# Performance work log

Hardware: AMD Instinct MI355X
Metric: run time of the kernel (lower is better)

The kernel has to match this reference:

```python
import jax, jax.numpy as jnp
import numpy as np

H = 16  # heads
D = 1024  # hidden
HD = D // H
FF = 4096
EPS = 1e-12


def _linear_params(key, d_in, d_out):
    k1, k2 = jax.random.split(key)
    bound = 1.0 / np.sqrt(d_in)
    W = jax.random.uniform(k1, (d_in, d_out), minval=-bound, maxval=bound, dtype=jnp.float32)
    b = jax.random.uniform(k2, (d_out,), minval=-bound, maxval=bound, dtype=jnp.float32)
    return W, b


def setup_inputs() -> dict:
    key = jax.random.key(0)
    ks = jax.random.split(key, 8)
    x = jax.random.normal(ks[0], (4, 2048, D), dtype=jnp.float32)
    mask = jnp.ones((4, 1, 1, 2048), dtype=jnp.int32)
    Wq, bq = _linear_params(ks[1], D, D)
    Wk, bk = _linear_params(ks[2], D, D)
    Wv, bv = _linear_params(ks[3], D, D)
    Wo, bo = _linear_params(ks[4], D, D)
    W1, b1 = _linear_params(ks[5], D, FF)
    W2, b2 = _linear_params(ks[6], FF, D)
    g1 = jnp.ones((D,), jnp.float32); be1 = jnp.zeros((D,), jnp.float32)
    g2 = jnp.ones((D,), jnp.float32); be2 = jnp.zeros((D,), jnp.float32)
    return {"x": x, "mask": mask,
            "Wq": Wq, "bq": bq, "Wk": Wk, "bk": bk, "Wv": Wv, "bv": bv,
            "Wo": Wo, "bo": bo, "W1": W1, "b1": b1, "W2": W2, "b2": b2,
            "g1": g1, "be1": be1, "g2": g2, "be2": be2}


def _layernorm(x, g, b):
    mu = jnp.mean(x, axis=-1, keepdims=True)
    var = jnp.mean(jnp.square(x - mu), axis=-1, keepdims=True)
    return (x - mu) / jnp.sqrt(var + EPS) * g + b


def reference(x, mask, Wq, bq, Wk, bk, Wv, bv, Wo, bo, W1, b1, W2, b2, g1, be1, g2, be2):
    B, L, _ = x.shape
    h = _layernorm(x, g1, be1)
    # [B, H, L, HD]
    q = (h @ Wq + bq).reshape(B, L, H, HD).transpose(0, 2, 1, 3)
    k = (h @ Wk + bk).reshape(B, L, H, HD).transpose(0, 2, 1, 3)
    v = (h @ Wv + bv).reshape(B, L, H, HD).transpose(0, 2, 1, 3)
    scores = jnp.einsum('bhqd,bhkd->bhqk', q, k) / np.sqrt(HD).astype(np.float32)
    scores = jnp.where(mask == 0, jnp.float32(-1e9), scores)
    attn = jax.nn.softmax(scores, axis=-1)  # dropout = identity (eval mode)
    out = jnp.einsum('bhqk,bhkd->bhqd', attn, v)
    out = out.transpose(0, 2, 1, 3).reshape(B, L, D)
    x = x + (out @ Wo + bo)
    h = _layernorm(x, g2, be2)
    ff = jax.nn.gelu(h @ W1 + b1, approximate=False) @ W2 + b2
    return x + ff
```

## Files before the change

### kernel.cpp

```cpp
#include <hip/hip_runtime.h>
#include <stdint.h>

#define D_MODEL 1024
#define NHEAD   16
#define HDIM    64
#define FFDIM   4096
#define BATCH   4
#define SEQ     2048
#define ROWS    (BATCH*SEQ)

typedef unsigned short u16;
typedef __bf16 bf16_t;
typedef bf16_t bf16x8 __attribute__((ext_vector_type(8)));
typedef float  f32x4  __attribute__((ext_vector_type(4)));
typedef float  f32x16 __attribute__((ext_vector_type(16)));

#define SCQ 0.18033688011112042f

__device__ __forceinline__ u16 f2bf(float f) {
  union { float f; unsigned u; } v; v.f = f;
  unsigned r = v.u + 0x7fffu + ((v.u >> 16) & 1u);
  return (u16)(r >> 16);
}

__device__ __forceinline__ void gl2lds16(const void* g, void* l) {
  __builtin_amdgcn_global_load_lds((const __attribute__((address_space(1))) void*)g,
                                   (__attribute__((address_space(3))) void*)l, 16, 0, 0);
}

#define MFMA_BF16(a, b, c) __builtin_amdgcn_mfma_f32_16x16x32_bf16((a), (b), (c), 0, 0, 0)
#define MFMA32(a, b, c)    __builtin_amdgcn_mfma_f32_32x32x16_bf16((a), (b), (c), 0, 0, 0)
#define EXP2(x) __builtin_amdgcn_exp2f(x)

__device__ __forceinline__ bf16x8 mk8(unsigned a, unsigned b, unsigned c, unsigned d) {
  union { unsigned u[4]; bf16x8 v; } t;
  t.u[0] = a; t.u[1] = b; t.u[2] = c; t.u[3] = d;
  return t.v;
}

__global__ __launch_bounds__(256) void ln_kernel(const float* __restrict__ x,
                                                 const float* __restrict__ g,
                                                 const float* __restrict__ be,
                                                 u16* __restrict__ out) {
  __shared__ float red[10];
  int row = blockIdx.x;
  int t = threadIdx.x;
  const float* xr = x + (size_t)row * D_MODEL;
  float4 xv = ((const float4*)xr)[t];
  float s  = xv.x + xv.y + xv.z + xv.w;
  float s2 = xv.x*xv.x + xv.y*xv.y + xv.z*xv.z + xv.w*xv.w;
  for (int d = 32; d > 0; d >>= 1) { s += __shfl_down(s, d); s2 += __shfl_down(s2, d); }
  int wid = t >> 6;
  if ((t & 63) == 0) { red[wid*2] = s; red[wid*2+1] = s2; }
  __syncthreads();
  if (t == 0) {
    float a = 0.f, b2 = 0.f;
    for (int i = 0; i < 4; ++i) { a += red[i*2]; b2 += red[i*2+1]; }
    red[8] = a; red[9] = b2;
  }
  __syncthreads();
  float mu  = red[8] * (1.0f / D_MODEL);
  float var = red[9] * (1.0f / D_MODEL) - mu*mu;
  float rstd = rsqrtf(var + 1e-12f);
  float4 gv = ((const float4*)g)[t];
  float4 bv = ((const float4*)be)[t];
  unsigned long long o =
      (unsigned long long)f2bf((xv.x - mu) * rstd * gv.x + bv.x)
    | ((unsigned long long)f2bf((xv.y - mu) * rstd * gv.y + bv.y) << 16)
    | ((unsigned long long)f2bf((xv.z - mu) * rstd * gv.z + bv.z) << 32)
    | ((unsigned long long)f2bf((xv.w - mu) * rstd * gv.w + bv.w) << 48);
  ((unsigned long long*)out)[(size_t)row * (D_MODEL/4) + t] = o;
}

__global__ __launch_bounds__(256) void wt_kernel(const float* __restrict__ W,
                                                 u16* __restrict__ Wt, int K, int N) {
  __shared__ float tile[32][33];
  int n0 = blockIdx.x * 32, k0 = blockIdx.y * 32;
  int tx = threadIdx.x & 31, ty = threadIdx.x >> 5;
  #pragma unroll
  for (int i = 0; i < 4; ++i) {
    int k = ty + i*8;
    tile[k][tx] = W[(size_t)(k0 + k) * N + n0 + tx];
  }
  __syncthreads();
  #pragma unroll
  for (int i = 0; i < 4; ++i) {
    int n = ty + i*8;
    Wt[(size_t)(n0 + n) * K + k0 + tx] = f2bf(tile[tx][n]);
  }
}

__global__ __launch_bounds__(256) void vtrans_kernel(const u16* __restrict__ vb,
                                                     u16* __restrict__ vt) {
  __shared__ __align__(16) u16 tile[64][80];
  int kb = blockIdx.x * 64;
  int bh = blockIdx.y;
  int b = bh >> 4, h = bh & 15;
  int t = threadIdx.x;
  int key = t >> 2, dq = (t & 3) * 16;
  const u16* src = vb + (size_t)b*SEQ*D_MODEL + (size_t)(kb+key)*D_MODEL + h*HDIM + dq;
  *(bf16x8*)&tile[key][dq]     = *(const bf16x8*)(src);
  *(bf16x8*)&tile[key][dq + 8] = *(const bf16x8*)(src + 8);
  __syncthreads();
  int w = t >> 6, lane = t & 63;
  int kq = w * 16;
  u16 vals[16];
  #pragma unroll
  for (int e = 0; e < 16; ++e) vals[e] = tile[kq + e][lane];
  u16* dst = vt + (size_t)bh * HDIM * SEQ + (size_t)lane * SEQ + kb + kq;
  *(bf16x8*)dst       = *(const bf16x8*)&vals[0];
  *(bf16x8*)(dst + 8) = *(const bf16x8*)&vals[8];
}

__device__ __forceinline__ float gelu_f(float v) {
  return 0.5f * v * (1.0f + erff(v * 0.70710678118654752f));
}

template<int EPI>
__global__ __launch_bounds__(512, 2) void gemm256(const u16* __restrict__ A,
                                                  const u16* __restrict__ Bt,
                                                  const float* __restrict__ bias,
                                                  const float* __restrict__ resid,
                                                  void* __restrict__ outp,
                                                  int M, int N, int K,
                                                  const float* __restrict__ bias2,
                                                  const float* __restrict__ bias3,
                                                  void* __restrict__ out2,
                                                  void* __restrict__ out3) {
  __shared__ __align__(16) u16 sA[3][128*64];
  __shared__ __align__(16) u16 sB[3][256*64];
  const int tid = threadIdx.x;
  const int lane = tid & 63, w = tid >> 6;
  const int r = lane & 15, kg = lane >> 4, r7 = r & 7;
  const int wr = w >> 2, wc = w & 3;

  const int gx = gridDim.x;
  const int nwg = gx * gridDim.y;
  const int orig = blockIdx.y * gx + blockIdx.x;
  const int lid = (orig & 7) * (nwg >> 3) + (orig >> 3);
  const int bm = lid / gx, bn = lid % gx;

  const int NT = K >> 6;

  size_t offA[2], offB[4];
  #pragma unroll
  for (int u = 0; u < 2; ++u) {
    int slot = u*512 + tid;
    int row = slot >> 3, g = slot & 7;
    offA[u] = (size_t)(bm*128 + row) * K + ((g ^ (row & 7)) * 8);
  }
  #pragma unroll
  for (int u = 0; u < 4; ++u) {
    int slot = u*512 + tid;
    int row = slot >> 3, g = slot & 7;
    offB[u] = (size_t)(bn*256 + row) * K + ((g ^ (row & 7)) * 8);
  }

  f32x4 acc[4][4];
  #pragma unroll
  for (int m = 0; m < 4; ++m)
    #pragma unroll
    for (int n = 0; n < 4; ++n) acc[m][n] = f32x4{0.f, 0.f, 0.f, 0.f};

  const float* bsel = bias;
  u16* osel = (u16*)outp;
  int bnl = bn;
  float qscale = 1.0f;
  if (EPI == 3) {
    int sec = bn >> 2;
    bsel = (sec == 0) ? bias : (sec == 1 ? bias2 : bias3);
    osel = (u16*)((sec == 0) ? outp : (sec == 1 ? out2 : out3));
    if (sec == 0) qscale = SCQ;
    bnl = bn & 3;
  }
  float bv4[4];
  #pragma unroll
  for (int n = 0; n < 4; ++n) bv4[n] = bsel[bnl*256 + wc*64 + n*16 + r];

  auto load_frags = [&](bf16x8 (&aa)[4], bf16x8 (&bb)[4], int bbuf, int sl) {
    #pragma unroll
    for (int m = 0; m < 4; ++m)
      aa[m] = *(const bf16x8*)&sA[bbuf][(wr*64 + m*16 + r)*64 + (((sl*4 + kg) ^ r7) * 8)];
    #pragma unroll
    for (int n = 0; n < 4; ++n)
      bb[n] = *(const bf16x8*)&sB[bbuf][(wc*64 + n*16 + r)*64 + (((sl*4 + kg) ^ r7) * 8)];
  };
  auto mfma16 = [&](bf16x8 (&aa)[4], bf16x8 (&bb)[4]) {
    __builtin_amdgcn_s_setprio(1);
    #pragma unroll
    for (int m = 0; m < 4; ++m)
      #pragma unroll
      for (int n = 0; n < 4; ++n)
        acc[m][n] = MFMA_BF16(aa[m], bb[n], acc[m][n]);
    __builtin_amdgcn_s_setprio(0);
  };

  #pragma unroll
  for (int u = 0; u < 2; ++u) gl2lds16(A  + offA[u],      &sA[0][(u*512+tid)*8]);
  #pragma unroll
  for (int u = 0; u < 4; ++u) gl2lds16(Bt + offB[u],      &sB[0][(u*512+tid)*8]);
  #pragma unroll
  for (int u = 0; u < 2; ++u) gl2lds16(A  + offA[u] + 64, &sA[1][(u*512+tid)*8]);
  #pragma unroll
  for (int u = 0; u < 4; ++u) gl2lds16(Bt + offB[u] + 64, &sB[1][(u*512+tid)*8]);
  asm volatile("s_waitcnt vmcnt(6)" ::: "memory");
  __builtin_amdgcn_s_barrier();

  bf16x8 a0[4], b0[4], a1[4], b1[4];
  load_frags(a0, b0, 0, 0);

  int buf = 0;
  for (int t = 0; t < NT - 1; ++t) {
    int nb = buf + 2; if (nb >= 3) nb -= 3;
    const bool pre = (t + 2 < NT);
    const size_t koff = (size_t)(t + 2) * 64;

    load_frags(a1, b1, buf, 1);
    if (pre) {
      gl2lds16(A  + offA[0] + koff, &sA[nb][(0*512+tid)*8]);
      gl2lds16(A  + offA[1] + koff, &sA[nb][(1*512+tid)*8]);
      gl2lds16(Bt + offB[0] + koff, &sB[nb][(0*512+tid)*8]);
      gl2lds16(Bt + offB[1] + koff, &sB[nb][(1*512+tid)*8]);
      gl2lds16(Bt + offB[2] + koff, &sB[nb][(2*512+tid)*8]);
      gl2lds16(Bt + offB[3] + koff, &sB[nb][(3*512+tid)*8]);
    }
    mfma16(a0, b0);
    asm volatile("s_waitcnt lgkmcnt(0)" ::: "memory");
    __builtin_amdgcn_sched_barrier(0);
    if (pre) asm volatile("s_waitcnt vmcnt(6)" ::: "memory");
    else     asm volatile("s_waitcnt vmcnt(0)" ::: "memory");
    __builtin_amdgcn_s_barrier();

    int bnext = buf + 1; if (bnext >= 3) bnext -= 3;
    load_frags(a0, b0, bnext, 0);
    mfma16(a1, b1);
    buf = bnext;
  }
  load_frags(a1, b1, buf, 1);
  mfma16(a0, b0);
  mfma16(a1, b1);

  const int orow = bm*128 + wr*64;
  const int ocol = (EPI == 3 ? bnl : bn)*256 + wc*64;
  const int ostride = (EPI == 3) ? 1024 : N;
  #pragma unroll
  for (int m = 0; m < 4; ++m) {
    #pragma unroll
    for (int n = 0; n < 4; ++n) {
      #pragma unroll
      for (int j = 0; j < 4; ++j) {
        int rr = orow + m*16 + kg*4 + j;
        int cc = ocol + n*16 + r;
        size_t idx = (size_t)rr * ostride + cc;
        float v = acc[m][n][j] + bv4[n];
        if (EPI == 0)       ((u16*)outp)[idx]   = f2bf(v);
        else if (EPI == 1)  ((float*)outp)[idx] = resid[idx] + v;
        else if (EPI == 2)  ((u16*)outp)[idx]   = f2bf(gelu_f(v));
        else                osel[idx]           = f2bf(v * qscale);
      }
    }
  }
}

__global__ __launch_bounds__(256, 4) void attn_kernel(const u16* __restrict__ qb,
                                                      const u16* __restrict__ kb,
                                                      const u16* __restrict__ vt,
                                                      const int* __restrict__ mask,
                                                      u16* __restrict__ ob) {
  __shared__ __align__(16) u16 sK[2][64*64];
  __shared__ __align__(16) u16 sV[2][64*64];
  __shared__ float sAl[4][32];
  __shared__ unsigned char sOkPart[256];
  __shared__ unsigned sTileOk;
  const float THR2 = 11.541560327111708f;
  int tid = threadIdx.x;
  int lane = tid & 63, w = tid >> 6;
  int l31 = lane & 31, hi = lane >> 5;
  int qt = blockIdx.x;
  int bh = blockIdx.y;
  int b = bh >> 4, h = bh & 15;
  size_t qkbase = (size_t)b * SEQ * D_MODEL + (size_t)h * HDIM;
  const u16* vtb = vt + (size_t)bh * HDIM * SEQ;
  const int* mrow = mask + b * SEQ;

  {
    int ok = 1;
    #pragma unroll
    for (int e = 0; e < 8; ++e) ok &= (mrow[tid*8 + e] != 0);
    sOkPart[tid] = (unsigned char)ok;
  }
  __syncthreads();
  if (w == 0) {
    int a = 0;
    if (lane < 32) {
      a = 1;
      #pragma unroll
      for (int e = 0; e < 8; ++e) a &= sOkPart[lane*8 + e];
    }
    unsigned long long bits = __ballot(a != 0);
    if (lane == 0) sTileOk = (unsigned)(bits & 0xffffffffu);
  }
  __syncthreads();
  const unsigned tileOkBits = sTileOk;

  const u16* qrow = qb + qkbase + (size_t)(qt*128 + w*32 + l31) * D_MODEL + hi*8;
  bf16x8 qf[4];
  #pragma unroll
  for (int dstep = 0; dstep < 4; ++dstep)
    qf[dstep] = *(const bf16x8*)(qrow + dstep*16);

  f32x16 oacc0, oacc1;
  #pragma unroll
  for (int e = 0; e < 16; ++e) { oacc0[e] = 0.f; oacc1[e] = 0.f; }
  float m_run = -1e30f;
  float lsum  = 0.f;

  int ch0 = w*64 + lane, ch1 = ch0 + 256;
  int row0 = ch0 >> 3, col0 = ((ch0 & 7) ^ (row0 & 7)) * 8;
  int row1 = ch1 >> 3, col1 = ((ch1 & 7) ^ (row1 & 7)) * 8;
  const u16* kp0 = kb + qkbase + (size_t)row0 * D_MODEL + col0;
  const u16* kp1 = kb + qkbase + (size_t)row1 * D_MODEL + col1;
  const u16* vp0 = vtb + (size_t)row0 * SEQ + col0;
  const u16* vp1 = vtb + (size_t)row1 * SEQ + col1;

  const int NT = SEQ / 64;

  gl2lds16(kp0, &sK[0][ch0*8]);
  gl2lds16(kp1, &sK[0][ch1*8]);
  gl2lds16(vp0, &sV[0][ch0*8]);
  gl2lds16(vp1, &sV[0][ch1*8]);
  kp0 += 64*D_MODEL; kp1 += 64*D_MODEL; vp0 += 64; vp1 += 64;

  for (int kt = 0; kt < NT; ++kt) {
    int cur = kt & 1;
    int key0 = kt * 64;
    if (kt + 1 < NT) {
      gl2lds16(kp0, &sK[cur^1][ch0*8]);
      gl2lds16(kp1, &sK[cur^1][ch1*8]);
      gl2lds16(vp0, &sV[cur^1][ch0*8]);
      gl2lds16(vp1, &sV[cur^1][ch1*8]);
      kp0 += 64*D_MODEL; kp1 += 64*D_MODEL; vp0 += 64; vp1 += 64;
      asm volatile("s_waitcnt vmcnt(4)" ::: "memory");
    } else {
      asm volatile("s_waitcnt vmcnt(0)" ::: "memory");
    }
    __builtin_amdgcn_s_barrier();

    const u16* Kt = sK[cur];
    const u16* Vt = sV[cur];

    f32x16 s0, s1;
    #pragma unroll
    for (int e = 0; e < 16; ++e) { s0[e] = 0.f; s1[e] = 0.f; }
    #pragma unroll
    for (int dstep = 0; dstep < 4; ++dstep) {
      int g = dstep*2 + hi;
      bf16x8 kf0 = *(const bf16x8*)&Kt[l31*64        + ((g ^ (l31 & 7)) * 8)];
      bf16x8 kf1 = *(const bf16x8*)&Kt[(32 + l31)*64 + ((g ^ ((32 + l31) & 7)) * 8)];
      s0 = MFMA32(kf0, qf[dstep], s0);
      s1 = MFMA32(kf1, qf[dstep], s1);
    }

    if (!((tileOkBits >> kt) & 1u)) {
      #pragma unroll
      for (int reg = 0; reg < 16; ++reg) {
        int kr = (reg & 3) + 8*(reg >> 2) + 4*hi;
        if (!mrow[key0 + kr])      s0[reg] = -1e9f;
        if (!mrow[key0 + 32 + kr]) s1[reg] = -1e9f;
      }
    }

    float tm = s0[0];
    #pragma unroll
    for (int e = 1; e < 16; ++e) tm = fmaxf(tm, s0[e]);
    #pragma unroll
    for (int e = 0; e < 16; ++e) tm = fmaxf(tm, s1[e]);
    tm = fmaxf(tm, __shfl_xor(tm, 32));

    if (__any(tm > m_run + THR2)) {
      float mn = fmaxf(m_run, tm);
      float al = EXP2(m_run - mn);
      m_run = mn;
      lsum *= al;
      if (lane < 32) sAl[w][lane] = al;
      asm volatile("s_waitcnt lgkmcnt(0)" ::: "memory");
      #pragma unroll
      for (int reg = 0; reg < 16; ++reg) {
        float a2 = sAl[w][(reg & 3) + 8*(reg >> 2) + 4*hi];
        oacc0[reg] *= a2; oacc1[reg] *= a2;
      }
    }

    #pragma unroll
    for (int e = 0; e < 16; ++e) {
      s0[e] = EXP2(s0[e] - m_run); lsum += s0[e];
      s1[e] = EXP2(s1[e] - m_run); lsum += s1[e];
    }

    unsigned wa, wb, wc, wd, we, wf, wg, wh;
#define CVTPK(dst, lo_, hi_) asm("v_cvt_pk_bf16_f32 %0, %1, %2" : "=v"(dst) : "v"(lo_), "v"(hi_))
    CVTPK(wa, s0[0],  s0[1]);  CVTPK(wb, s0[2],  s0[3]);
    CVTPK(wc, s0[4],  s0[5]);  CVTPK(wd, s0[6],  s0[7]);
    CVTPK(we, s0[8],  s0[9]);  CVTPK(wf, s0[10], s0[11]);
    CVTPK(wg, s0[12], s0[13]); CVTPK(wh, s0[14], s0[15]);
    asm volatile("v_permlane32_swap_b32 %0, %1" : "+v"(wc), "+v"(wa));
    asm volatile("v_permlane32_swap_b32 %0, %1" : "+v"(wd), "+v"(wb));
    asm volatile("v_permlane32_swap_b32 %0, %1" : "+v"(wg), "+v"(we));
    asm volatile("v_permlane32_swap_b32 %0, %1" : "+v"(wh), "+v"(wf));
    bf16x8 pa0 = mk8(wa, wb, wc, wd);
    bf16x8 pa1 = mk8(we, wf, wg, wh);
    CVTPK(wa, s1[0],  s1[1]);  CVTPK(wb, s1[2],  s1[3]);
    CVTPK(wc, s1[4],  s1[5]);  CVTPK(wd, s1[6],  s1[7]);
    CVTPK(we, s1[8],  s1[9]);  CVTPK(wf, s1[10], s1[11]);
    CVTPK(wg, s1[12], s1[13]); CVTPK(wh, s1[14], s1[15]);
    asm volatile("v_permlane32_swap_b32 %0, %1" : "+v"(wc), "+v"(wa));
    asm volatile("v_permlane32_swap_b32 %0, %1" : "+v"(wd), "+v"(wb));
    asm volatile("v_permlane32_swap_b32 %0, %1" : "+v"(wg), "+v"(we));
    asm volatile("v_permlane32_swap_b32 %0, %1" : "+v"(wh), "+v"(wf));
    bf16x8 pa2 = mk8(wa, wb, wc, wd);
    bf16x8 pa3 = mk8(we, wf, wg, wh);
#undef CVTPK

    int r0 = l31, r1 = 32 + l31;
    #pragma unroll
    for (int kstep = 0; kstep < 4; ++kstep) {
      int g = kstep*2 + hi;
      bf16x8 vf0 = *(const bf16x8*)&Vt[r0*64 + ((g ^ (r0 & 7)) * 8)];
      bf16x8 vf1 = *(const bf16x8*)&Vt[r1*64 + ((g ^ (r1 & 7)) * 8)];
      bf16x8 pk = (kstep == 0) ? pa0 : (kstep == 1) ? pa1 : (kstep == 2) ? pa2 : pa3;
      oacc0 = MFMA32(pk, vf0, oacc0);
      oacc1 = MFMA32(pk, vf1, oacc1);
    }
    __builtin_amdgcn_s_barrier();
  }

  float lsumT = lsum + __shfl_xor(lsum, 32);
  if (lane < 32) sAl[w][lane] = 1.0f / lsumT;
  asm volatile("s_waitcnt lgkmcnt(0)" ::: "memory");
  #pragma unroll
  for (int reg = 0; reg < 16; ++reg) {
    int qr = (reg & 3) + 8*(reg >> 2) + 4*hi;
    float rc = sAl[w][qr];
    int qg = qt*128 + w*32 + qr;
    size_t base2 = (size_t)(b*SEQ + qg) * D_MODEL + h*HDIM + l31;
    ob[base2]      = f2bf(oacc0[reg] * rc);
    ob[base2 + 32] = f2bf(oacc1[reg] * rc);
  }
}

extern "C" void kernel_launch(void* const* d_in, const int* in_sizes, int n_in,
                              void* d_out, int out_size, void* d_ws, size_t ws_size,
                              hipStream_t stream) {
  const float* x   = (const float*)d_in[0];
  const int*  mask = (const int*)d_in[1];
  const float* Wq = (const float*)d_in[2];  const float* bq = (const float*)d_in[3];
  const float* Wk = (const float*)d_in[4];  const float* bk = (const float*)d_in[5];
  const float* Wv = (const float*)d_in[6];  const float* bv = (const float*)d_in[7];
  const float* Wo = (const float*)d_in[8];  const float* bo = (const float*)d_in[9];
  const float* W1 = (const float*)d_in[10]; const float* b1 = (const float*)d_in[11];
  const float* W2 = (const float*)d_in[12]; const float* b2 = (const float*)d_in[13];
  const float* g1 = (const float*)d_in[14]; const float* be1 = (const float*)d_in[15];
  const float* g2 = (const float*)d_in[16]; const float* be2 = (const float*)d_in[17];

  const size_t MB = 1u << 20;
  char* ws = (char*)d_ws;
  u16*  hln  = (u16*)(ws);
  u16*  vt   = (u16*)(ws);
  u16*  qb   = (u16*)(ws + 16*MB);
  u16*  kb   = (u16*)(ws + 32*MB);
  u16*  vb   = (u16*)(ws + 48*MB);
  u16*  attn = (u16*)(ws + 64*MB);
  u16*  ff1  = (u16*)(ws + 16*MB);
  float* x2  = (float*)(ws + 80*MB);
  u16*  WqkvT= (u16*)(ws + 112*MB);
  u16*  WqT  = WqkvT;
  u16*  WkT  = (u16*)(ws + 114*MB);
  u16*  WvT  = (u16*)(ws + 116*MB);
  u16*  WoT  = (u16*)(ws + 118*MB);
  u16*  W1T  = (u16*)(ws + 120*MB);
  u16*  W2T  = (u16*)(ws + 128*MB);

  dim3 tb(256);
  wt_kernel<<<dim3(1024/32, 1024/32), tb, 0, stream>>>(Wq, WqT, 1024, 1024);
  wt_kernel<<<dim3(1024/32, 1024/32), tb, 0, stream>>>(Wk, WkT, 1024, 1024);
  wt_kernel<<<dim3(1024/32, 1024/32), tb, 0, stream>>>(Wv, WvT, 1024, 1024);
  wt_kernel<<<dim3(1024/32, 1024/32), tb, 0, stream>>>(Wo, WoT, 1024, 1024);
  wt_kernel<<<dim3(4096/32, 1024/32), tb, 0, stream>>>(W1, W1T, 1024, 4096);
  wt_kernel<<<dim3(1024/32, 4096/32), tb, 0, stream>>>(W2, W2T, 4096, 1024);

  ln_kernel<<<ROWS, tb, 0, stream>>>(x, g1, be1, hln);

  dim3 gb(512);
  gemm256<3><<<dim3(3072/256, ROWS/128), gb, 0, stream>>>(hln, WqkvT, bq, nullptr, qb,
                                                          ROWS, 3072, 1024,
                                                          bk, bv, kb, vb);

  vtrans_kernel<<<dim3(SEQ/64, BATCH*NHEAD), tb, 0, stream>>>(vb, vt);

  attn_kernel<<<dim3(SEQ/128, BATCH*NHEAD), tb, 0, stream>>>(qb, kb, vt, mask, attn);

  gemm256<1><<<dim3(1024/256, ROWS/128), gb, 0, stream>>>(attn, WoT, bo, x, x2,
                                                          ROWS, 1024, 1024,
                                                          nullptr, nullptr, nullptr, nullptr);

  ln_kernel<<<ROWS, tb, 0, stream>>>(x2, g2, be2, hln);

  gemm256<2><<<dim3(4096/256, ROWS/128), gb, 0, stream>>>(hln, W1T, b1, nullptr, ff1,
                                                          ROWS, 4096, 1024,
                                                          nullptr, nullptr, nullptr, nullptr);

  gemm256<1><<<dim3(1024/256, ROWS/128), gb, 0, stream>>>(ff1, W2T, b2, x2, (float*)d_out,
                                                          ROWS, 1024, 4096,
                                                          nullptr, nullptr, nullptr, nullptr);
}
```

Baseline: 387.8 us.

## Halve GEMM K-tile to 32 and raise occupancy to 4 blocks per CU

Shrinks the shared-memory K tile from 64 to 32 bf16 elements, which halves LDS use per block, adjusts the XOR swizzle to the narrower rows, and raises launch bounds to allow 4 blocks per CU. The pipeline drops the double-buffered register fragments and uses one fragment load followed by 16 MFMAs per tile, with a barrier on every 32-wide step. More resident blocks are meant to hide latency better. In exchange there are twice as many barriers and waits, less MFMA work per sync, and register pressure under a 4-block bound that may cause spills.

```diff
diff --git a/kernel.cpp b/kernel.cpp
--- a/kernel.cpp
+++ b/kernel.cpp
@@ -117,7 +117,7 @@
 }
 
 template<int EPI>
-__global__ __launch_bounds__(512, 2) void gemm256(const u16* __restrict__ A,
+__global__ __launch_bounds__(512, 4) void gemm256(const u16* __restrict__ A,
                                                   const u16* __restrict__ Bt,
                                                   const float* __restrict__ bias,
                                                   const float* __restrict__ resid,
@@ -127,11 +127,12 @@
                                                   const float* __restrict__ bias3,
                                                   void* __restrict__ out2,
                                                   void* __restrict__ out3) {
-  __shared__ __align__(16) u16 sA[3][128*64];
-  __shared__ __align__(16) u16 sB[3][256*64];
+  __shared__ __align__(16) u16 sA[3][128*32];
+  __shared__ __align__(16) u16 sB[3][256*32];
   const int tid = threadIdx.x;
   const int lane = tid & 63, w = tid >> 6;
-  const int r = lane & 15, kg = lane >> 4, r7 = r & 7;
+  const int r = lane & 15, kg = lane >> 4;
+  const int rs = (r >> 1) & 3;
   const int wr = w >> 2, wc = w & 3;
 
   const int gx = gridDim.x;
@@ -140,20 +141,18 @@
   const int lid = (orig & 7) * (nwg >> 3) + (orig >> 3);
   const int bm = lid / gx, bn = lid % gx;
 
-  const int NT = K >> 6;
-
-  size_t offA[2], offB[4];
+  const int NT = K >> 5;
+
+  size_t offA, offB[2];
+  {
+    int row = tid >> 2, g = tid & 3;
+    offA = (size_t)(bm*128 + row) * K + ((g ^ ((row >> 1) & 3)) * 8);
+  }
   #pragma unroll
   for (int u = 0; u < 2; ++u) {
     int slot = u*512 + tid;
-    int row = slot >> 3, g = slot & 7;
-    offA[u] = (size_t)(bm*128 + row) * K + ((g ^ (row & 7)) * 8);
-  }
-  #pragma unroll
-  for (int u = 0; u < 4; ++u) {
-    int slot = u*512 + tid;
-    int row = slot >> 3, g = slot & 7;
-    offB[u] = (size_t)(bn*256 + row) * K + ((g ^ (row & 7)) * 8);
+    int row = slot >> 2, g = slot & 3;
+    offB[u] = (size_t)(bn*256 + row) * K + ((g ^ ((row >> 1) & 3)) * 8);
   }
 
   f32x4 acc[4][4];
@@ -177,68 +176,48 @@
   #pragma unroll
   for (int n = 0; n < 4; ++n) bv4[n] = bsel[bnl*256 + wc*64 + n*16 + r];
 
-  auto load_frags = [&](bf16x8 (&aa)[4], bf16x8 (&bb)[4], int bbuf, int sl) {
+  auto stage = [&](int bbuf, int t) {
+    const size_t koff = (size_t)t * 32;
+    gl2lds16(A  + offA    + koff, &sA[bbuf][tid*8]);
+    gl2lds16(Bt + offB[0] + koff, &sB[bbuf][tid*8]);
+    gl2lds16(Bt + offB[1] + koff, &sB[bbuf][(512+tid)*8]);
+  };
+
+  stage(0, 0);
+  stage(1, 1);
+  asm volatile("s_waitcnt vmcnt(3)" ::: "memory");
+  __builtin_amdgcn_s_barrier();
+
+  int buf = 0;
+  for (int t = 0; t < NT; ++t) {
+    const bool pre = (t + 2 < NT);
+    int nb = buf + 2; if (nb >= 3) nb -= 3;
+
+    if (pre) stage(nb, t + 2);
+
+    bf16x8 af[4], bfr[4];
     #pragma unroll
     for (int m = 0; m < 4; ++m)
-      aa[m] = *(const bf16x8*)&sA[bbuf][(wr*64 + m*16 + r)*64 + (((sl*4 + kg) ^ r7) * 8)];
+      af[m]  = *(const bf16x8*)&sA[buf][(wr*64 + m*16 + r)*32 + ((kg ^ rs) * 8)];
     #pragma unroll
     for (int n = 0; n < 4; ++n)
-      bb[n] = *(const bf16x8*)&sB[bbuf][(wc*64 + n*16 + r)*64 + (((sl*4 + kg) ^ r7) * 8)];
-  };
-  auto mfma16 = [&](bf16x8 (&aa)[4], bf16x8 (&bb)[4]) {
+      bfr[n] = *(const bf16x8*)&sB[buf][(wc*64 + n*16 + r)*32 + ((kg ^ rs) * 8)];
+
+    asm volatile("s_waitcnt lgkmcnt(0)" ::: "memory");
+    __builtin_amdgcn_sched_barrier(0);
     __builtin_amdgcn_s_setprio(1);
     #pragma unroll
     for (int m = 0; m < 4; ++m)
       #pragma unroll
       for (int n = 0; n < 4; ++n)
-        acc[m][n] = MFMA_BF16(aa[m], bb[n], acc[m][n]);
+        acc[m][n] = MFMA_BF16(af[m], bfr[n], acc[m][n]);
     __builtin_amdgcn_s_setprio(0);
-  };
-
-  #pragma unroll
-  for (int u = 0; u < 2; ++u) gl2lds16(A  + offA[u],      &sA[0][(u*512+tid)*8]);
-  #pragma unroll
-  for (int u = 0; u < 4; ++u) gl2lds16(Bt + offB[u],      &sB[0][(u*512+tid)*8]);
-  #pragma unroll
-  for (int u = 0; u < 2; ++u) gl2lds16(A  + offA[u] + 64, &sA[1][(u*512+tid)*8]);
-  #pragma unroll
-  for (int u = 0; u < 4; ++u) gl2lds16(Bt + offB[u] + 64, &sB[1][(u*512+tid)*8]);
-  asm volatile("s_waitcnt vmcnt(6)" ::: "memory");
-  __builtin_amdgcn_s_barrier();
-
-  bf16x8 a0[4], b0[4], a1[4], b1[4];
-  load_frags(a0, b0, 0, 0);
-
-  int buf = 0;
-  for (int t = 0; t < NT - 1; ++t) {
-    int nb = buf + 2; if (nb >= 3) nb -= 3;
-    const bool pre = (t + 2 < NT);
-    const size_t koff = (size_t)(t + 2) * 64;
-
-    load_frags(a1, b1, buf, 1);
-    if (pre) {
-      gl2lds16(A  + offA[0] + koff, &sA[nb][(0*512+tid)*8]);
-      gl2lds16(A  + offA[1] + koff, &sA[nb][(1*512+tid)*8]);
-      gl2lds16(Bt + offB[0] + koff, &sB[nb][(0*512+tid)*8]);
-      gl2lds16(Bt + offB[1] + koff, &sB[nb][(1*512+tid)*8]);
-      gl2lds16(Bt + offB[2] + koff, &sB[nb][(2*512+tid)*8]);
-      gl2lds16(Bt + offB[3] + koff, &sB[nb][(3*512+tid)*8]);
-    }
-    mfma16(a0, b0);
-    asm volatile("s_waitcnt lgkmcnt(0)" ::: "memory");
-    __builtin_amdgcn_sched_barrier(0);
-    if (pre) asm volatile("s_waitcnt vmcnt(6)" ::: "memory");
+
+    if (pre) asm volatile("s_waitcnt vmcnt(3)" ::: "memory");
     else     asm volatile("s_waitcnt vmcnt(0)" ::: "memory");
     __builtin_amdgcn_s_barrier();
-
-    int bnext = buf + 1; if (bnext >= 3) bnext -= 3;
-    load_frags(a0, b0, bnext, 0);
-    mfma16(a1, b1);
-    buf = bnext;
-  }
-  load_frags(a1, b1, buf, 1);
-  mfma16(a0, b0);
-  mfma16(a1, b1);
+    buf += 1; if (buf >= 3) buf -= 3;
+  }
 
   const int orow = bm*128 + wr*64;
   const int ocol = (EPI == 3 ? bnl : bn)*256 + wc*64;
```

Result: slower. 444.4 us (+14.6%).
